# Kernel tuning notes

Hardware: AMD Instinct MI355X
Metric: run time of the kernel (lower is better)

The kernel has to match this reference:

```python
import jax, jax.numpy as jnp
import numpy as np

T, B, U = 64, 2048, 1024


def setup_inputs() -> dict:
    key = jax.random.key(0)
    ks = jax.random.split(key, 7)
    inputs = jax.random.normal(ks[0], (T, B, 1), dtype=jnp.float32)
    x1_0 = jax.random.normal(ks[1], (B, 1), dtype=jnp.float32)
    x2_0 = jax.random.normal(ks[2], (B, 1), dtype=jnp.float32)
    c0 = jax.random.normal(ks[3], (B, U), dtype=jnp.float32)
    kernel = jax.random.normal(ks[4], (1, 2 * U), dtype=jnp.float32) * 0.05
    # orthogonal-ish recurrent kernel, scaled for stability
    recurrent_kernel = jax.random.normal(ks[5], (U, 2 * U), dtype=jnp.float32) * (1.0 / np.sqrt(U))
    # unit_forget_bias: ones for the f gate, zeros for the c gate
    bias = jnp.concatenate([jnp.ones((U,), jnp.float32), jnp.zeros((U,), jnp.float32)])
    output_kernel = jax.random.normal(ks[6], (U, 1), dtype=jnp.float32) * 0.05
    return {"inputs": inputs, "x1_0": x1_0, "x2_0": x2_0, "c0": c0,
            "kernel": kernel, "recurrent_kernel": recurrent_kernel,
            "bias": bias, "output_kernel": output_kernel}


def reference(inputs, x1_0, x2_0, c0, kernel, recurrent_kernel, bias, output_kernel):
    U = c0.shape[-1]
    Kf, Kc = kernel[:, :U], kernel[:, U:2 * U]          # [1,U] each
    Rf, Rc = recurrent_kernel[:, :U], recurrent_kernel[:, U:2 * U]  # [U,U]
    bf, bc = bias[:U], bias[U:2 * U]

    def step(carry, inp):
        x1, x2, h = carry                 # x1,x2: [B,1]; h (= c_{t-1}): [B,U]
        x_f = h @ Rf + x1 @ Kf + bf       # [B,U]
        x_c = h @ Rc + x1 @ Kc + bc       # [B,U]
        f = jax.nn.sigmoid(x_f)
        c = f * h + (1.0 - f) * jnp.tanh(x_c)
        x1_new = x1 + x2                  # double-integrator position update
        x2_new = x2 + inp * (c @ output_kernel)  # velocity driven by scalar input * readout
        return (x1_new, x2_new, c), x1_new

    _, outputs = jax.lax.scan(step, (x1_0, x2_0, c0), inputs)
    return outputs  # [T, B, 1]
```

## Files before the change

### kernel.cpp

```cpp
#include <hip/hip_runtime.h>
#include <hip/hip_bf16.h>

#define T_STEPS 64
#define B_DIM 2048
#define U_DIM 1024

#define BM 128
#define BU 64
#define BK 32
#define KITERS (U_DIM / BK)
#define NSTG 4

typedef __attribute__((ext_vector_type(8))) _Float16 h8;
typedef __attribute__((ext_vector_type(4))) float f4;

__device__ __forceinline__ void async_cp16(const _Float16* g, _Float16* l) {
    __builtin_amdgcn_global_load_lds((const __attribute__((address_space(1))) void*)g,
                                     (__attribute__((address_space(3))) void*)l,
                                     16, 0, 0);
}


__global__ void transpose_R(const float* __restrict__ R, _Float16* __restrict__ Rt) {
    __shared__ float tile[32][33];
    int nb = blockIdx.x * 32;
    int kb = blockIdx.y * 32;
    int tx = threadIdx.x, ty = threadIdx.y;
    #pragma unroll
    for (int i = ty; i < 32; i += 8)
        tile[i][tx] = R[(size_t)(kb + i) * (2 * U_DIM) + nb + tx];
    __syncthreads();
    #pragma unroll
    for (int i = ty; i < 32; i += 8)
        Rt[(size_t)(nb + i) * U_DIM + kb + tx] = (_Float16)tile[tx][i];
}

__global__ void init_state(const float* __restrict__ c0, _Float16* __restrict__ h0,
                           float* __restrict__ y) {
    int i = blockIdx.x * 256 + threadIdx.x;
    h0[i] = (_Float16)c0[i];
    if (i < 3 * B_DIM) y[i] = 0.f;
}

__global__ __launch_bounds__(256, 1) void gemm_step(
    const _Float16* __restrict__ hA, _Float16* __restrict__ hB,
    const _Float16* __restrict__ Rt,
    const float* __restrict__ x1_0, const float* __restrict__ x2_0,
    float* __restrict__ x1w,
    float* __restrict__ x2w,
    const float* __restrict__ kern, const float* __restrict__ bias,
    const float* __restrict__ okern,
    float* __restrict__ y,
    const float* __restrict__ inputs,
    float* __restrict__ out,
    int t)
{
    __shared__ __align__(16) _Float16 lS[4][NSTG][4096];
    __shared__ float x1s[BM];

    const int tid    = threadIdx.x;
    const int wid    = tid >> 6;
    const int lane   = tid & 63;
    const int lane15 = lane & 15;
    const int quad   = lane >> 4;
    const int u0     = blockIdx.x * BU;
    const int b0     = blockIdx.y * BM;
    const int wrow   = (wid >> 1) * 64;
    const int wcol   = (wid & 1) * 32;

    if (tid < BM) {
        const int b = b0 + tid;
        float x1n, x2n;
        if (t == 0) {
            x1n = x1_0[b];
            x2n = x2_0[b];
        } else {
            const int rd = (t + 1) & 1;
            const float x1p = x1w[rd * B_DIM + b];
            const float x2p = x2w[rd * B_DIM + b];
            const float yp  = y[((t + 2) % 3) * B_DIM + b];
            const float ip  = inputs[(size_t)(t - 1) * B_DIM + b];
            x1n = x1p + x2p;
            x2n = x2p + ip * yp;
        }
        x1s[tid] = x1n;
        if (blockIdx.x == 0) {
            const int wr = t & 1;
            x1w[wr * B_DIM + b] = x1n;
            x2w[wr * B_DIM + b] = x2n;
            if (t > 0) out[(size_t)(t - 1) * B_DIM + b] = x1n;
            y[((t + 1) % 3) * B_DIM + b] = 0.f;
        }
    }

    float kf[2], kc[2], bf_[2], bc_[2], ok_[2];
    #pragma unroll
    for (int nt = 0; nt < 2; ++nt) {
        const int u = u0 + wcol + nt * 16 + lane15;
        kf[nt] = kern[u];
        kc[nt] = kern[U_DIM + u];
        bf_[nt] = bias[u];
        bc_[nt] = bias[U_DIM + u];
        ok_[nt] = okern[u];
    }
    _Float16 hv[4][2][4];
    #pragma unroll
    for (int mt = 0; mt < 4; ++mt)
        #pragma unroll
        for (int nt = 0; nt < 2; ++nt)
            #pragma unroll
            for (int reg = 0; reg < 4; ++reg)
                hv[mt][nt][reg] = hA[(size_t)(b0 + wrow + mt * 16 + quad * 4 + reg) * U_DIM
                                     + u0 + wcol + nt * 16 + lane15];

    const int srow  = lane >> 2;
    const int schnk = ((lane & 3) ^ (srow & 3)) * 8;
    auto stage = [&](int st, int kt) {
        const int k0 = kt * BK;
        #pragma unroll
        for (int j = 0; j < 4; ++j)
            async_cp16(hA + (size_t)(b0 + wrow + j * 16 + srow) * U_DIM + k0 + schnk,
                       &lS[wid][st][j * 512]);
        #pragma unroll
        for (int j = 0; j < 2; ++j) {
            async_cp16(Rt + (size_t)(u0 + wcol + j * 16 + srow) * U_DIM + k0 + schnk,
                       &lS[wid][st][2048 + j * 512]);
            async_cp16(Rt + (size_t)(U_DIM + u0 + wcol + j * 16 + srow) * U_DIM + k0 + schnk,
                       &lS[wid][st][3072 + j * 512]);
        }
    };
    stage(0, 0);
    stage(1, 1);
    stage(2, 2);

    f4 accF[4][2], accC[4][2];
    #pragma unroll
    for (int mt = 0; mt < 4; ++mt)
        #pragma unroll
        for (int nt = 0; nt < 2; ++nt) {
            accF[mt][nt] = (f4){0.f, 0.f, 0.f, 0.f};
            accC[mt][nt] = (f4){0.f, 0.f, 0.f, 0.f};
        }

    const int sw = (quad ^ (lane15 & 3)) * 8;
    auto body = [&](int kt) {
        const int st = kt & 3;
        h8 af[4], bff[2], bfc[2];
        #pragma unroll
        for (int mt = 0; mt < 4; ++mt)
            af[mt] = *(const h8*)&lS[wid][st][mt * 512 + lane15 * 32 + sw];
        #pragma unroll
        for (int nt = 0; nt < 2; ++nt) {
            bff[nt] = *(const h8*)&lS[wid][st][2048 + nt * 512 + lane15 * 32 + sw];
            bfc[nt] = *(const h8*)&lS[wid][st][3072 + nt * 512 + lane15 * 32 + sw];
        }
        #pragma unroll
        for (int mt = 0; mt < 4; ++mt)
            #pragma unroll
            for (int nt = 0; nt < 2; ++nt) {
                accF[mt][nt] = __builtin_amdgcn_mfma_f32_16x16x32_f16(af[mt], bff[nt], accF[mt][nt], 0, 0, 0);
                accC[mt][nt] = __builtin_amdgcn_mfma_f32_16x16x32_f16(af[mt], bfc[nt], accC[mt][nt], 0, 0, 0);
            }
    };

    for (int kt = 0; kt < KITERS - 2; ++kt) {
        __builtin_amdgcn_s_waitcnt(0x4F70);
        body(kt);
        if (kt + 3 < KITERS) stage((kt + 3) & 3, kt + 3);
    }
    __builtin_amdgcn_s_waitcnt(0x0F78);
    body(KITERS - 2);
    __builtin_amdgcn_s_waitcnt(0x0F70);
    body(KITERS - 1);

    __syncthreads();

    _Float16* lC = &lS[0][0][0];
    float* ycur = y + (t % 3) * B_DIM;
    #pragma unroll
    for (int mt = 0; mt < 4; ++mt) {
        const int rlb = wrow + mt * 16 + quad * 4;
        float psum[4] = {0.f, 0.f, 0.f, 0.f};
        #pragma unroll
        for (int nt = 0; nt < 2; ++nt) {
            const int ul = wcol + nt * 16 + lane15;
            #pragma unroll
            for (int reg = 0; reg < 4; ++reg) {
                const int rl = rlb + reg;
                const float x1 = x1s[rl];
                const float xf = accF[mt][nt][reg] + x1 * kf[nt] + bf_[nt];
                const float xc = accC[mt][nt][reg] + x1 * kc[nt] + bc_[nt];
                const float fg = 1.f / (1.f + __expf(-xf));
                const float th = 1.f - 2.f / (1.f + __expf(2.f * xc));
                const float cv = fg * (float)hv[mt][nt][reg] + (1.f - fg) * th;
                lC[rl * 72 + ul] = (_Float16)cv;
                psum[reg] += cv * ok_[nt];
            }
        }
        #pragma unroll
        for (int reg = 0; reg < 4; ++reg) {
            float s = psum[reg];
            s += __shfl_xor(s, 1);
            s += __shfl_xor(s, 2);
            s += __shfl_xor(s, 4);
            s += __shfl_xor(s, 8);
            if (lane15 == 0) atomicAdd(&ycur[b0 + rlb + reg], s);
        }
    }

    __syncthreads();
    #pragma unroll
    for (int j = 0; j < 4; ++j) {
        const int idx = j * 256 + tid;
        const int row = idx >> 3;
        const int col = idx & 7;
        *(uint4*)&hB[(size_t)(b0 + row) * U_DIM + u0 + col * 8] =
            *(const uint4*)&lC[row * 72 + col * 8];
    }
}

__global__ void finish(const float* __restrict__ x1w1, const float* __restrict__ x2w1,
                       float* __restrict__ out_last) {
    const int i = blockIdx.x * 256 + threadIdx.x;
    out_last[i] = x1w1[i] + x2w1[i];
}

extern "C" void kernel_launch(void* const* d_in, const int* in_sizes, int n_in,
                              void* d_out, int out_size, void* d_ws, size_t ws_size,
                              hipStream_t stream) {
    const float* inputs = (const float*)d_in[0];
    const float* x1_0   = (const float*)d_in[1];
    const float* x2_0   = (const float*)d_in[2];
    const float* c0     = (const float*)d_in[3];
    const float* kern   = (const float*)d_in[4];
    const float* rker   = (const float*)d_in[5];
    const float* bias   = (const float*)d_in[6];
    const float* okern  = (const float*)d_in[7];
    float* out = (float*)d_out;

    _Float16* Rt = (_Float16*)d_ws;
    _Float16* h0 = Rt + (size_t)2 * U_DIM * U_DIM;
    _Float16* h1 = h0 + (size_t)B_DIM * U_DIM;
    float* y   = (float*)(h1 + (size_t)B_DIM * U_DIM);
    float* x1w = y + 3 * B_DIM;
    float* x2w = x1w + 2 * B_DIM;

    transpose_R<<<dim3(64, 32), dim3(32, 8), 0, stream>>>(rker, Rt);
    init_state<<<dim3(B_DIM * U_DIM / 256), dim3(256), 0, stream>>>(c0, h0, y);

    _Float16* hcur = h0;
    _Float16* hnxt = h1;
    for (int t = 0; t < T_STEPS; ++t) {
        gemm_step<<<dim3(U_DIM / BU, B_DIM / BM), dim3(256), 0, stream>>>(
            hcur, hnxt, Rt, x1_0, x2_0, x1w, x2w, kern, bias, okern, y,
            inputs, out, t);
        _Float16* tmp = hcur; hcur = hnxt; hnxt = tmp;
    }
    finish<<<dim3(B_DIM / 256), dim3(256), 0, stream>>>(
        x1w + B_DIM, x2w + B_DIM, out + (size_t)(T_STEPS - 1) * B_DIM);
}
```

Measured before the change: 1.526 ms.

## Replace per-step launches with persistent kernel using group barriers and LDS-resident weights

Replaces the 64 per-timestep GEMM launches with one persistent kernel of 256 blocks. Each block owns 256 batch rows by 32 units and keeps its slice of the recurrent weights resident in LDS for all steps, so only the hidden state is streamed each step. Steps are separated by a software barrier over atomic counters, and since the batch rows are independent, only the 32 blocks sharing a batch slice wait on each other. The block checks whether its group sits on a single XCD and skips the release fence if so. This removes launch overhead and repeated weight reloads, but relies on all 256 blocks being co-resident, and the fence skip relies on same-XCD cache coherence.

After: 1.720 ms. +12.7%, slower.

```diff
diff --git a/kernel.cpp b/kernel.cpp
--- a/kernel.cpp
+++ b/kernel.cpp
@@ -4,12 +4,7 @@
 #define T_STEPS 64
 #define B_DIM 2048
 #define U_DIM 1024
-
-#define BM 128
-#define BU 64
-#define BK 32
-#define KITERS (U_DIM / BK)
-#define NSTG 4
+#define KITERS 32
 
 typedef __attribute__((ext_vector_type(8))) _Float16 h8;
 typedef __attribute__((ext_vector_type(4))) float f4;
@@ -36,193 +31,225 @@
 }
 
 __global__ void init_state(const float* __restrict__ c0, _Float16* __restrict__ h0,
-                           float* __restrict__ y) {
+                           float* __restrict__ y, unsigned* __restrict__ bar) {
     int i = blockIdx.x * 256 + threadIdx.x;
     h0[i] = (_Float16)c0[i];
     if (i < 3 * B_DIM) y[i] = 0.f;
-}
-
-__global__ __launch_bounds__(256, 1) void gemm_step(
-    const _Float16* __restrict__ hA, _Float16* __restrict__ hB,
+    if (i < 256) bar[i] = 0u;
+}
+
+__global__ __launch_bounds__(256, 1) void persist(
+    _Float16* __restrict__ h0, _Float16* __restrict__ h1,
     const _Float16* __restrict__ Rt,
     const float* __restrict__ x1_0, const float* __restrict__ x2_0,
-    float* __restrict__ x1w,
-    float* __restrict__ x2w,
     const float* __restrict__ kern, const float* __restrict__ bias,
     const float* __restrict__ okern,
-    float* __restrict__ y,
+    float* y,
     const float* __restrict__ inputs,
     float* __restrict__ out,
-    int t)
+    unsigned* bar)
 {
-    __shared__ __align__(16) _Float16 lS[4][NSTG][4096];
-    __shared__ float x1s[BM];
+    __shared__ __align__(16) _Float16 lB[2][2][KITERS][512];
+    __shared__ __align__(16) _Float16 lA[4][2][4][512];
 
     const int tid    = threadIdx.x;
     const int wid    = tid >> 6;
     const int lane   = tid & 63;
     const int lane15 = lane & 15;
     const int quad   = lane >> 4;
-    const int u0     = blockIdx.x * BU;
-    const int b0     = blockIdx.y * BM;
-    const int wrow   = (wid >> 1) * 64;
-    const int wcol   = (wid & 1) * 32;
-
-    if (tid < BM) {
-        const int b = b0 + tid;
-        float x1n, x2n;
-        if (t == 0) {
-            x1n = x1_0[b];
-            x2n = x2_0[b];
-        } else {
-            const int rd = (t + 1) & 1;
-            const float x1p = x1w[rd * B_DIM + b];
-            const float x2p = x2w[rd * B_DIM + b];
-            const float yp  = y[((t + 2) % 3) * B_DIM + b];
-            const float ip  = inputs[(size_t)(t - 1) * B_DIM + b];
-            x1n = x1p + x2p;
-            x2n = x2p + ip * yp;
-        }
-        x1s[tid] = x1n;
-        if (blockIdx.x == 0) {
-            const int wr = t & 1;
-            x1w[wr * B_DIM + b] = x1n;
-            x2w[wr * B_DIM + b] = x2n;
-            if (t > 0) out[(size_t)(t - 1) * B_DIM + b] = x1n;
-            y[((t + 1) % 3) * B_DIM + b] = 0.f;
-        }
+    const int bid    = blockIdx.x;
+    const int b0     = (bid & 7) * 256;
+    const int u0     = (bid >> 3) * 32;
+    const bool ub0   = (bid >> 3) == 0;
+    const int wrow   = wid * 64;
+    const int srow   = lane >> 2;
+    const int schnk  = ((lane & 3) ^ (srow & 3)) * 8;
+    const int sw     = (quad ^ (lane15 & 3)) * 8;
+    const int myb    = b0 + tid;
+    unsigned* ctr   = &bar[(bid & 7) * 32];
+    unsigned* xmask = &bar[(bid & 7) * 32 + 8];
+
+    #pragma unroll
+    for (int gate = 0; gate < 2; ++gate)
+        #pragma unroll
+        for (int nt = 0; nt < 2; ++nt)
+            #pragma unroll
+            for (int i = 0; i < 8; ++i) {
+                const int kt = wid + i * 4;
+                async_cp16(Rt + (size_t)(gate * U_DIM + u0 + nt * 16 + srow) * U_DIM + kt * 32 + schnk,
+                           &lB[gate][nt][kt][0]);
+            }
+
+    int* flag = (int*)&lA[0][0][0][0];
+    if (tid == 0) {
+        const unsigned xcc = (unsigned)__builtin_amdgcn_s_getreg(63508) & 31u;
+        __hip_atomic_fetch_or(xmask, 1u << xcc, __ATOMIC_RELAXED, __HIP_MEMORY_SCOPE_AGENT);
+        __hip_atomic_fetch_add(ctr, 1u, __ATOMIC_RELAXED, __HIP_MEMORY_SCOPE_AGENT);
+        while (__hip_atomic_load(ctr, __ATOMIC_RELAXED, __HIP_MEMORY_SCOPE_AGENT) < 32u)
+            __builtin_amdgcn_s_sleep(2);
+        const unsigned m = __hip_atomic_load(xmask, __ATOMIC_RELAXED, __HIP_MEMORY_SCOPE_AGENT);
+        *flag = (__popc(m) == 1) ? 1 : 0;
     }
+    __syncthreads();
+    const bool xcd_pure = (*flag != 0);
 
     float kf[2], kc[2], bf_[2], bc_[2], ok_[2];
     #pragma unroll
     for (int nt = 0; nt < 2; ++nt) {
-        const int u = u0 + wcol + nt * 16 + lane15;
-        kf[nt] = kern[u];
-        kc[nt] = kern[U_DIM + u];
-        bf_[nt] = bias[u];
-        bc_[nt] = bias[U_DIM + u];
+        const int u = u0 + nt * 16 + lane15;
+        kf[nt]  = kern[u];        kc[nt]  = kern[U_DIM + u];
+        bf_[nt] = bias[u];        bc_[nt] = bias[U_DIM + u];
         ok_[nt] = okern[u];
     }
-    _Float16 hv[4][2][4];
-    #pragma unroll
-    for (int mt = 0; mt < 4; ++mt)
-        #pragma unroll
-        for (int nt = 0; nt < 2; ++nt)
-            #pragma unroll
-            for (int reg = 0; reg < 4; ++reg)
-                hv[mt][nt][reg] = hA[(size_t)(b0 + wrow + mt * 16 + quad * 4 + reg) * U_DIM
-                                     + u0 + wcol + nt * 16 + lane15];
-
-    const int srow  = lane >> 2;
-    const int schnk = ((lane & 3) ^ (srow & 3)) * 8;
-    auto stage = [&](int st, int kt) {
-        const int k0 = kt * BK;
-        #pragma unroll
-        for (int j = 0; j < 4; ++j)
-            async_cp16(hA + (size_t)(b0 + wrow + j * 16 + srow) * U_DIM + k0 + schnk,
-                       &lS[wid][st][j * 512]);
-        #pragma unroll
-        for (int j = 0; j < 2; ++j) {
-            async_cp16(Rt + (size_t)(u0 + wcol + j * 16 + srow) * U_DIM + k0 + schnk,
-                       &lS[wid][st][2048 + j * 512]);
-            async_cp16(Rt + (size_t)(U_DIM + u0 + wcol + j * 16 + srow) * U_DIM + k0 + schnk,
-                       &lS[wid][st][3072 + j * 512]);
-        }
-    };
-    stage(0, 0);
-    stage(1, 1);
-    stage(2, 2);
-
-    f4 accF[4][2], accC[4][2];
-    #pragma unroll
-    for (int mt = 0; mt < 4; ++mt)
-        #pragma unroll
-        for (int nt = 0; nt < 2; ++nt) {
-            accF[mt][nt] = (f4){0.f, 0.f, 0.f, 0.f};
-            accC[mt][nt] = (f4){0.f, 0.f, 0.f, 0.f};
-        }
-
-    const int sw = (quad ^ (lane15 & 3)) * 8;
-    auto body = [&](int kt) {
-        const int st = kt & 3;
-        h8 af[4], bff[2], bfc[2];
+
+    float x1r = x1_0[myb];
+    float x2r = x2_0[myb];
+
+    __builtin_amdgcn_s_waitcnt(0x0F70);
+    __syncthreads();
+
+    _Float16* hA_ = h0;
+    _Float16* hB_ = h1;
+    _Float16* lC  = &lA[0][0][0][0];
+    float*    x1s = (float*)&lA[2][1][0][0];
+
+    #pragma unroll 1
+    for (int t = 0; t < T_STEPS; ++t) {
+        if (t > 0) {
+            const float ip = inputs[(size_t)(t - 1) * B_DIM + myb];
+            const float yp = __hip_atomic_load(&y[((t + 2) % 3) * B_DIM + myb],
+                                               __ATOMIC_RELAXED, __HIP_MEMORY_SCOPE_AGENT);
+            x1r = x1r + x2r;
+            x2r = x2r + ip * yp;
+        }
+        if (ub0) {
+            if (t > 0) out[(size_t)(t - 1) * B_DIM + myb] = x1r;
+            if (t == T_STEPS - 1)
+                out[(size_t)(T_STEPS - 1) * B_DIM + myb] = x1r + x2r;
+            else
+                __hip_atomic_store(&y[((t + 1) % 3) * B_DIM + myb], 0.f,
+                                   __ATOMIC_RELAXED, __HIP_MEMORY_SCOPE_AGENT);
+        }
+        if (t == T_STEPS - 1) break;
+
+        _Float16 hv[4][2][4];
         #pragma unroll
         for (int mt = 0; mt < 4; ++mt)
-            af[mt] = *(const h8*)&lS[wid][st][mt * 512 + lane15 * 32 + sw];
-        #pragma unroll
-        for (int nt = 0; nt < 2; ++nt) {
-            bff[nt] = *(const h8*)&lS[wid][st][2048 + nt * 512 + lane15 * 32 + sw];
-            bfc[nt] = *(const h8*)&lS[wid][st][3072 + nt * 512 + lane15 * 32 + sw];
-        }
+            #pragma unroll
+            for (int nt = 0; nt < 2; ++nt)
+                #pragma unroll
+                for (int reg = 0; reg < 4; ++reg)
+                    hv[mt][nt][reg] = hA_[(size_t)(b0 + wrow + mt * 16 + quad * 4 + reg) * U_DIM
+                                          + u0 + nt * 16 + lane15];
+
+        auto stageA = [&](int st, int kt) {
+            const int k0 = kt * 32;
+            #pragma unroll
+            for (int j = 0; j < 4; ++j)
+                async_cp16(hA_ + (size_t)(b0 + wrow + j * 16 + srow) * U_DIM + k0 + schnk,
+                           &lA[wid][st][j][0]);
+        };
+
+        f4 accF[4][2], accC[4][2];
         #pragma unroll
         for (int mt = 0; mt < 4; ++mt)
             #pragma unroll
             for (int nt = 0; nt < 2; ++nt) {
-                accF[mt][nt] = __builtin_amdgcn_mfma_f32_16x16x32_f16(af[mt], bff[nt], accF[mt][nt], 0, 0, 0);
-                accC[mt][nt] = __builtin_amdgcn_mfma_f32_16x16x32_f16(af[mt], bfc[nt], accC[mt][nt], 0, 0, 0);
-            }
-    };
-
-    for (int kt = 0; kt < KITERS - 2; ++kt) {
-        __builtin_amdgcn_s_waitcnt(0x4F70);
-        body(kt);
-        if (kt + 3 < KITERS) stage((kt + 3) & 3, kt + 3);
+                accF[mt][nt] = (f4){0.f, 0.f, 0.f, 0.f};
+                accC[mt][nt] = (f4){0.f, 0.f, 0.f, 0.f};
+            }
+
+        auto body = [&](int kt) {
+            const int st = kt & 1;
+            h8 af[4], bff[2], bfc[2];
+            #pragma unroll
+            for (int mt = 0; mt < 4; ++mt)
+                af[mt] = *(const h8*)&lA[wid][st][mt][lane15 * 32 + sw];
+            #pragma unroll
+            for (int nt = 0; nt < 2; ++nt) {
+                bff[nt] = *(const h8*)&lB[0][nt][kt][lane15 * 32 + sw];
+                bfc[nt] = *(const h8*)&lB[1][nt][kt][lane15 * 32 + sw];
+            }
+            #pragma unroll
+            for (int mt = 0; mt < 4; ++mt)
+                #pragma unroll
+                for (int nt = 0; nt < 2; ++nt) {
+                    accF[mt][nt] = __builtin_amdgcn_mfma_f32_16x16x32_f16(af[mt], bff[nt], accF[mt][nt], 0, 0, 0);
+                    accC[mt][nt] = __builtin_amdgcn_mfma_f32_16x16x32_f16(af[mt], bfc[nt], accC[mt][nt], 0, 0, 0);
+                }
+        };
+
+        stageA(0, 0);
+        stageA(1, 1);
+        for (int kt = 0; kt < KITERS - 2; ++kt) {
+            __builtin_amdgcn_s_waitcnt(0x0F74);
+            body(kt);
+            stageA(kt & 1, kt + 2);
+        }
+        __builtin_amdgcn_s_waitcnt(0x0F74);
+        body(KITERS - 2);
+        __builtin_amdgcn_s_waitcnt(0x0F70);
+        body(KITERS - 1);
+
+        __syncthreads();
+        x1s[tid] = x1r;
+        __syncthreads();
+
+        float* ycur = y + (t % 3) * B_DIM;
+        #pragma unroll
+        for (int mt = 0; mt < 4; ++mt) {
+            const int rlb = wrow + mt * 16 + quad * 4;
+            float psum[4] = {0.f, 0.f, 0.f, 0.f};
+            #pragma unroll
+            for (int nt = 0; nt < 2; ++nt) {
+                const int ul = nt * 16 + lane15;
+                #pragma unroll
+                for (int reg = 0; reg < 4; ++reg) {
+                    const int rl = rlb + reg;
+                    const float x1 = x1s[rl];
+                    const float xf = accF[mt][nt][reg] + x1 * kf[nt] + bf_[nt];
+                    const float xc = accC[mt][nt][reg] + x1 * kc[nt] + bc_[nt];
+                    const float fg = 1.f / (1.f + __expf(-xf));
+                    const float th = 1.f - 2.f / (1.f + __expf(2.f * xc));
+                    const float cv = fg * (float)hv[mt][nt][reg] + (1.f - fg) * th;
+                    lC[rl * 40 + ul] = (_Float16)cv;
+                    psum[reg] += cv * ok_[nt];
+                }
+            }
+            #pragma unroll
+            for (int reg = 0; reg < 4; ++reg) {
+                float s = psum[reg];
+                s += __shfl_xor(s, 1);
+                s += __shfl_xor(s, 2);
+                s += __shfl_xor(s, 4);
+                s += __shfl_xor(s, 8);
+                if (lane15 == 0) atomicAdd(&ycur[b0 + rlb + reg], s);
+            }
+        }
+
+        __syncthreads();
+        #pragma unroll
+        for (int j = 0; j < 4; ++j) {
+            const int idx = j * 256 + tid;
+            const int row = idx >> 2;
+            const int col = idx & 3;
+            *(uint4*)&hB_[(size_t)(b0 + row) * U_DIM + u0 + col * 8] =
+                *(const uint4*)&lC[row * 40 + col * 8];
+        }
+
+        { _Float16* tmp = hA_; hA_ = hB_; hB_ = tmp; }
+
+        if (!xcd_pure) __builtin_amdgcn_fence(__ATOMIC_RELEASE, "agent");
+        __syncthreads();
+        if (tid == 0) {
+            __hip_atomic_fetch_add(ctr, 1u, __ATOMIC_RELAXED, __HIP_MEMORY_SCOPE_AGENT);
+            while (__hip_atomic_load(ctr, __ATOMIC_RELAXED, __HIP_MEMORY_SCOPE_AGENT)
+                   < 32u * (unsigned)(t + 2))
+                __builtin_amdgcn_s_sleep(2);
+        }
+        __syncthreads();
+        __builtin_amdgcn_fence(__ATOMIC_ACQUIRE, "agent");
     }
-    __builtin_amdgcn_s_waitcnt(0x0F78);
-    body(KITERS - 2);
-    __builtin_amdgcn_s_waitcnt(0x0F70);
-    body(KITERS - 1);
-
-    __syncthreads();
-
-    _Float16* lC = &lS[0][0][0];
-    float* ycur = y + (t % 3) * B_DIM;
-    #pragma unroll
-    for (int mt = 0; mt < 4; ++mt) {
-        const int rlb = wrow + mt * 16 + quad * 4;
-        float psum[4] = {0.f, 0.f, 0.f, 0.f};
-        #pragma unroll
-        for (int nt = 0; nt < 2; ++nt) {
-            const int ul = wcol + nt * 16 + lane15;
-            #pragma unroll
-            for (int reg = 0; reg < 4; ++reg) {
-                const int rl = rlb + reg;
-                const float x1 = x1s[rl];
-                const float xf = accF[mt][nt][reg] + x1 * kf[nt] + bf_[nt];
-                const float xc = accC[mt][nt][reg] + x1 * kc[nt] + bc_[nt];
-                const float fg = 1.f / (1.f + __expf(-xf));
-                const float th = 1.f - 2.f / (1.f + __expf(2.f * xc));
-                const float cv = fg * (float)hv[mt][nt][reg] + (1.f - fg) * th;
-                lC[rl * 72 + ul] = (_Float16)cv;
-                psum[reg] += cv * ok_[nt];
-            }
-        }
-        #pragma unroll
-        for (int reg = 0; reg < 4; ++reg) {
-            float s = psum[reg];
-            s += __shfl_xor(s, 1);
-            s += __shfl_xor(s, 2);
-            s += __shfl_xor(s, 4);
-            s += __shfl_xor(s, 8);
-            if (lane15 == 0) atomicAdd(&ycur[b0 + rlb + reg], s);
-        }
-    }
-
-    __syncthreads();
-    #pragma unroll
-    for (int j = 0; j < 4; ++j) {
-        const int idx = j * 256 + tid;
-        const int row = idx >> 3;
-        const int col = idx & 7;
-        *(uint4*)&hB[(size_t)(b0 + row) * U_DIM + u0 + col * 8] =
-            *(const uint4*)&lC[row * 72 + col * 8];
-    }
-}
-
-__global__ void finish(const float* __restrict__ x1w1, const float* __restrict__ x2w1,
-                       float* __restrict__ out_last) {
-    const int i = blockIdx.x * 256 + threadIdx.x;
-    out_last[i] = x1w1[i] + x2w1[i];
 }
 
 extern "C" void kernel_launch(void* const* d_in, const int* in_sizes, int n_in,
@@ -241,21 +268,11 @@
     _Float16* Rt = (_Float16*)d_ws;
     _Float16* h0 = Rt + (size_t)2 * U_DIM * U_DIM;
     _Float16* h1 = h0 + (size_t)B_DIM * U_DIM;
-    float* y   = (float*)(h1 + (size_t)B_DIM * U_DIM);
-    float* x1w = y + 3 * B_DIM;
-    float* x2w = x1w + 2 * B_DIM;
+    float* y = (float*)(h1 + (size_t)B_DIM * U_DIM);
+    unsigned* bar = (unsigned*)(y + 3 * B_DIM);
 
     transpose_R<<<dim3(64, 32), dim3(32, 8), 0, stream>>>(rker, Rt);
-    init_state<<<dim3(B_DIM * U_DIM / 256), dim3(256), 0, stream>>>(c0, h0, y);
-
-    _Float16* hcur = h0;
-    _Float16* hnxt = h1;
-    for (int t = 0; t < T_STEPS; ++t) {
-        gemm_step<<<dim3(U_DIM / BU, B_DIM / BM), dim3(256), 0, stream>>>(
-            hcur, hnxt, Rt, x1_0, x2_0, x1w, x2w, kern, bias, okern, y,
-            inputs, out, t);
-        _Float16* tmp = hcur; hcur = hnxt; hnxt = tmp;
-    }
-    finish<<<dim3(B_DIM / 256), dim3(256), 0, stream>>>(
-        x1w + B_DIM, x2w + B_DIM, out + (size_t)(T_STEPS - 1) * B_DIM);
-}
+    init_state<<<dim3(B_DIM * U_DIM / 256), dim3(256), 0, stream>>>(c0, h0, y, bar);
+    persist<<<dim3(256), dim3(256), 0, stream>>>(h0, h1, Rt, x1_0, x2_0,
+                                                 kern, bias, okern, y, inputs, out, bar);
+}
```
